# Kernel tuning notes

Measured on AMD Instinct MI355X. Metric: run time of the kernel, lower is better.

The kernel has to match this reference:

```python
import jax, jax.numpy as jnp
import numpy as np

ANCHORS_ALL = np.array([[10.,13.],[16.,30.],[33.,23.],[30.,61.],[62.,45.],
                        [59.,119.],[116.,90.],[156.,198.],[373.,326.]], np.float32)
ANCHORS_MASK = [0, 1, 2]
NUM_CLASS = 80
BBOX_ATTRIB = 5 + NUM_CLASS
IGNORE_THRES = 0.7
EPS = 1e-12


def _iou_cxcywh(a, b):
    ax1, ax2 = a[..., 0] - a[..., 2] / 2, a[..., 0] + a[..., 2] / 2
    ay1, ay2 = a[..., 1] - a[..., 3] / 2, a[..., 1] + a[..., 3] / 2
    bx1, bx2 = b[..., 0] - b[..., 2] / 2, b[..., 0] + b[..., 2] / 2
    by1, by2 = b[..., 1] - b[..., 3] / 2, b[..., 1] + b[..., 3] / 2
    iw = jnp.clip(jnp.minimum(ax2, bx2) - jnp.maximum(ax1, bx1), 0.0)
    ih = jnp.clip(jnp.minimum(ay2, by2) - jnp.maximum(ay1, by1), 0.0)
    inter = iw * ih
    union = a[..., 2] * a[..., 3] + b[..., 2] * b[..., 3] - inter
    return inter / (union + 1e-16)


def _build_targets(pred_boxes, target, anchors_all, anchors, nH, nW):
    # vectorized version of the per-(batch, gt-box) python double loop
    nB, nT, _ = target.shape
    nA = anchors.shape[0]
    # emulate `break` on first all-zero target row via cumulative validity
    valid = jnp.cumprod((target.sum(-1) != 0).astype(jnp.int32), axis=1).astype(bool)  # [B,T]
    gx, gy = target[..., 1] * nW, target[..., 2] * nH
    gw, gh = target[..., 3] * nW, target[..., 4] * nH
    gi = jnp.clip(gx.astype(jnp.int32), 0, nW - 1)
    gj = jnp.clip(gy.astype(jnp.int32), 0, nH - 1)
    gt_boxes = jnp.stack([gx, gy, gw, gh], -1)                                    # [B,T,4]
    # IoU of every GT against every predicted box -> ignore mask for noobj
    ious = _iou_cxcywh(pred_boxes.reshape(nB, 1, -1, 4), gt_boxes[:, :, None, :])  # [B,T,P]
    ignore = (ious > IGNORE_THRES) & valid[..., None]
    noobj_mask = 1.0 - jnp.any(ignore, axis=1).reshape(nB, nA, nH, nW).astype(jnp.float32)
    # anchor matching on w/h only (both boxes centered at origin)
    aw, ah = anchors_all[:, 0], anchors_all[:, 1]                                  # [9]
    inter = jnp.minimum(gw[..., None], aw) * jnp.minimum(gh[..., None], ah)
    union = gw[..., None] * gh[..., None] + aw * ah - inter
    best = jnp.argmax(inter / (union + 1e-16), axis=-1)                            # [B,T]
    lut = -np.ones(len(ANCHORS_ALL), np.int32)
    lut[np.array(ANCHORS_MASK)] = np.arange(nA, dtype=np.int32)
    a_loc = jnp.asarray(lut)[best]
    write = valid & (a_loc >= 0)                # only GTs whose best anchor is in this head's mask
    a_loc = jnp.clip(a_loc, 0)
    b_idx = jnp.where(write, jnp.arange(nB)[:, None], nB)   # route masked-out writes to dummy row nB
    coord_v = jnp.sqrt(2.0 - target[..., 3] * target[..., 4])
    tw_v = jnp.log(gw / anchors[a_loc, 0] + 1e-16)
    th_v = jnp.log(gh / anchors[a_loc, 1] + 1e-16)
    cls_i = jnp.clip(target[..., 0].astype(jnp.int32), 0, NUM_CLASS - 1)

    def scat(vals):
        return jnp.zeros((nB + 1, nA, nH, nW), jnp.float32).at[b_idx, a_loc, gj, gi].set(vals)[:nB]

    obj_mask = scat(jnp.ones_like(gx))
    box_coord_mask = scat(coord_v)
    tx = scat(gx - gi)
    ty = scat(gy - gj)
    tw = scat(tw_v)
    th = scat(th_v)
    tcls = (jnp.zeros((nB + 1, nA, nH, nW, NUM_CLASS), jnp.float32)
            .at[b_idx, a_loc, gj, gi, cls_i].set(1.0)[:nB])
    return obj_mask, noobj_mask, box_coord_mask, obj_mask, tcls, tx, ty, tw, th


def _bce_sum(p, t):
    return -jnp.sum(t * jnp.log(p + EPS) + (1.0 - t) * jnp.log(1.0 - p + EPS))


def _forward(x, target, img_dim):
    nB, _, nH, nW = x.shape
    nA = len(ANCHORS_MASK)
    stride = img_dim / nH
    anchors_all = jnp.asarray(ANCHORS_ALL) / stride
    anchors = anchors_all[jnp.asarray(ANCHORS_MASK)]
    preds = x.reshape(nB, nA, BBOX_ATTRIB, nH, nW).transpose(0, 1, 3, 4, 2)  # [B,A,H,W,85]
    preds_xy = jax.nn.sigmoid(preds[..., :2])
    preds_wh = preds[..., 2:4]
    preds_conf = jax.nn.sigmoid(preds[..., 4])
    preds_cls = jax.nn.sigmoid(preds[..., 5:])
    mesh_xy = jnp.stack(jnp.meshgrid(jnp.arange(nW, dtype=jnp.float32),
                                     jnp.arange(nH, dtype=jnp.float32)), -1)  # [H,W,2] = (x,y)
    # decoded boxes are detached in the original (used only to build targets)
    pred_boxes = jnp.concatenate(
        [jax.lax.stop_gradient(preds_xy) + mesh_xy,
         jnp.exp(jax.lax.stop_gradient(preds_wh)) * anchors[None, :, None, None, :]], -1)
    tgt = jax.lax.stop_gradient(target)  # target.detach() in original
    (obj_mask, noobj_mask, box_coord_mask, tconf, tcls,
     tx, ty, tw, th) = _build_targets(pred_boxes, tgt, anchors_all, anchors, nH, nW)
    mse = lambda a, b: jnp.sum((a - b) ** 2)
    loss_x = mse(preds_xy[..., 0] * box_coord_mask, tx * box_coord_mask) / 2
    loss_y = mse(preds_xy[..., 1] * box_coord_mask, ty * box_coord_mask) / 2
    loss_w = mse(preds_wh[..., 0] * box_coord_mask, tw * box_coord_mask) / 2
    loss_h = mse(preds_wh[..., 1] * box_coord_mask, th * box_coord_mask) / 2
    loss_conf = (_bce_sum(preds_conf * obj_mask, obj_mask)
                 + _bce_sum(preds_conf * noobj_mask, jnp.zeros_like(preds_conf)))
    # BCE over cls entries of object cells only (sum reduction) == mask-weighted sum
    loss_cls = -jnp.sum(obj_mask[..., None] * (tcls * jnp.log(preds_cls + EPS)
                                               + (1.0 - tcls) * jnp.log(1.0 - preds_cls + EPS)))
    return loss_x + loss_y + loss_w + loss_h + loss_conf + loss_cls


def setup_inputs() -> dict:
    key = jax.random.key(0)
    k1, k2, k3, k4 = jax.random.split(key, 4)
    nB, nT = 16, 50
    x = jax.random.normal(k1, (nB, 3 * BBOX_ATTRIB, 76, 76), jnp.float32)
    cls = jnp.floor(jax.random.uniform(k2, (nB, nT, 1)) * NUM_CLASS)
    cxy = jax.random.uniform(k3, (nB, nT, 2), minval=0.05, maxval=0.95)
    wh = jax.random.uniform(k4, (nB, nT, 2), minval=0.02, maxval=0.4)
    target = jnp.concatenate([cls, cxy, wh], -1).astype(jnp.float32)
    return {"x": x, "target": target, "img_dim": 608}


def reference(x, target, img_dim):
    return _forward(x, target, img_dim)
```

## Files before the change

### kernel.cpp

```cpp
#include <hip/hip_runtime.h>

#define NBATCH 16
#define NTGT   50
#define NA     3
#define NH     76
#define NW     76
#define HW     (NH*NW)
#define NC     80
#define NATT   85
#define CELLS  (NA*HW)
#define CBLK   68
#define BPB    (CBLK + 1)
#define NPART  (BPB * NBATCH)

__device__ __constant__ float c_anchors[18] = {
  10.f,13.f, 16.f,30.f, 33.f,23.f, 30.f,61.f, 62.f,45.f,
  59.f,119.f, 116.f,90.f, 156.f,198.f, 373.f,326.f };

__device__ inline float read_dim(const void* p) {
  int iv = *(const int*)p;
  if (iv > 0 && iv < (1 << 24)) return (float)iv;
  return *(const float*)p;
}

__launch_bounds__(256)
__global__ void yolo_all(const float* __restrict__ x,
                         const float* __restrict__ tgt,
                         const void*  __restrict__ dimp,
                         float*       __restrict__ wsf) {
  __shared__ float4 sbox[NTGT];
  __shared__ float  sarea[NTGT];
  __shared__ int    skey[NTGT];
  __shared__ int    scl [NTGT];
  __shared__ int    snv;
  __shared__ float  sred[4];

  int b   = blockIdx.y;
  int bx  = blockIdx.x;
  int tid = threadIdx.x;
  float istride = (float)NH / read_dim(dimp);

  float gx = 0.f, gy = 0.f, gw = 0.f, gh = 0.f, w = 0.f, h = 0.f;
  int   gi = 0, gj = 0, a = 0, mykey = -1;
  if (tid < 64) {
    float cls = 0.f, cx = 0.f, cy = 0.f, s = 1.f;
    if (tid < NTGT) {
      const float* tr = tgt + (size_t)(b * NTGT + tid) * 5;
      cls = tr[0]; cx = tr[1]; cy = tr[2]; w = tr[3]; h = tr[4];
      s = cls + cx + cy + w + h;
    }
    unsigned long long mz = __ballot(tid < NTGT && s == 0.0f);
    int nv = mz ? (__ffsll(mz) - 1) : NTGT;

    gx = cx * NW; gy = cy * NH; gw = w * NW; gh = h * NH;
    gi = min(max((int)gx, 0), NW - 1);
    gj = min(max((int)gy, 0), NH - 1);

    float best_r = -1.0f; int best = 0;
    for (int k = 0; k < 9; k++) {
      float aw = c_anchors[2*k] * istride, ah = c_anchors[2*k+1] * istride;
      float inter = fminf(gw, aw) * fminf(gh, ah);
      float uni   = gw * gh + aw * ah - inter;
      float r = inter / (uni + 1e-16f);
      if (r > best_r) { best_r = r; best = k; }
    }
    a = (best < NA) ? best : 0;
    mykey = (tid < nv && best < NA) ? (a * HW + gj * NW + gi) : -1;

    if (tid < NTGT) {
      sbox[tid]  = make_float4(gx - gw*0.5f, gx + gw*0.5f,
                               gy - gh*0.5f, gy + gh*0.5f);
      sarea[tid] = gw * gh;
      skey[tid]  = mykey;
      scl [tid]  = min(max((int)cls, 0), NC - 1);
    }
    if (tid == 0) snv = nv;
  }
  __syncthreads();

  float loss = 0.0f;
  int nv = snv;

  if (bx < CBLK) {
    int cell = bx * 256 + tid;
    if (cell < CELLS) {
      int ca  = cell / HW;
      int rem = cell - ca * HW;
      int j   = rem / NW;
      int i   = rem - j * NW;
      const float* xb = x + ((size_t)(b * NA + ca) * NATT) * HW + rem;
      float px = xb[0*HW], py = xb[1*HW], pw = xb[2*HW], ph = xb[3*HW], pc = xb[4*HW];
      float spx   = 1.0f / (1.0f + __expf(-px));
      float spy   = 1.0f / (1.0f + __expf(-py));
      float sconf = 1.0f / (1.0f + __expf(-pc));
      float bw = __expf(pw) * c_anchors[2*ca]   * istride;
      float bh = __expf(ph) * c_anchors[2*ca+1] * istride;
      float bxc = spx + (float)i, byc = spy + (float)j;
      float ax1 = bxc - bw * 0.5f, ax2 = bxc + bw * 0.5f;
      float ay1 = byc - bh * 0.5f, ay2 = byc + bh * 0.5f;
      float areaA = bw * bh;

      bool ign = false;
      for (int t = 0; t < nv; t++) {
        float4 bb = sbox[t];
        float iw = fmaxf(fminf(ax2, bb.y) - fmaxf(ax1, bb.x), 0.0f);
        float ih = fmaxf(fminf(ay2, bb.w) - fmaxf(ay1, bb.z), 0.0f);
        float inter = iw * ih;
        float uni   = areaA + sarea[t] - inter + 1e-16f;
        ign = ign | (inter > 0.7f * uni);
      }
      if (!ign) loss = -__logf(1.0f - sconf + 1e-12f);
    }
  } else if (tid < 64 && mykey >= 0) {
    bool winner = true;
    unsigned cb0 = 0, cb1 = 0, cb2 = 0;
    for (int t2 = 0; t2 < nv; t2++) {
      if (skey[t2] == mykey) {
        if (t2 > tid) winner = false;
        int c = scl[t2];
        if (c < 32)      cb0 |= (1u << c);
        else if (c < 64) cb1 |= (1u << (c - 32));
        else             cb2 |= (1u << (c - 64));
      }
    }
    if (winner) {
      const float* xb = x + ((size_t)(b * NA + a) * NATT) * HW + gj * NW + gi;
      float px = xb[0*HW], py = xb[1*HW], pw = xb[2*HW], ph = xb[3*HW], pc = xb[4*HW];
      float spx   = 1.0f / (1.0f + __expf(-px));
      float spy   = 1.0f / (1.0f + __expf(-py));
      float sconf = 1.0f / (1.0f + __expf(-pc));
      float aw = c_anchors[2*a] * istride, ah = c_anchors[2*a+1] * istride;
      loss += -__logf(sconf + 1e-12f);
      float m  = sqrtf(2.0f - w * h);
      float dx = (spx - (gx - (float)gi)) * m;
      float dy = (spy - (gy - (float)gj)) * m;
      float dw = (pw  - __logf(gw / aw + 1e-16f)) * m;
      float dh = (ph  - __logf(gh / ah + 1e-16f)) * m;
      loss += 0.5f * (dx*dx + dy*dy + dw*dw + dh*dh);
      for (int c = 0; c < NC; c++) {
        float pv = 1.0f / (1.0f + __expf(-xb[(5 + c) * HW]));
        bool on = (c < 32) ? ((cb0 >> c) & 1u)
                : (c < 64) ? ((cb1 >> (c - 32)) & 1u)
                           : ((cb2 >> (c - 64)) & 1u);
        loss += on ? -__logf(pv + 1e-12f) : -__logf(1.0f - pv + 1e-12f);
      }
    }
  }

  for (int off = 32; off > 0; off >>= 1) loss += __shfl_down(loss, off, 64);
  int wave = tid >> 6, lane = tid & 63;
  if (lane == 0) sred[wave] = loss;
  __syncthreads();
  if (tid == 0) wsf[b * BPB + bx] = sred[0] + sred[1] + sred[2] + sred[3];
}

__global__ void yolo_reduce(const float* __restrict__ wsf,
                            float*       __restrict__ out) {
  __shared__ float sred[4];
  int tid = threadIdx.x;
  float s = 0.0f;
  for (int i = tid; i < NPART; i += 256) s += wsf[i];
  for (int off = 32; off > 0; off >>= 1) s += __shfl_down(s, off, 64);
  int wave = tid >> 6, lane = tid & 63;
  if (lane == 0) sred[wave] = s;
  __syncthreads();
  if (tid == 0) out[0] = sred[0] + sred[1] + sred[2] + sred[3];
}

extern "C" void kernel_launch(void* const* d_in, const int* in_sizes, int n_in,
                              void* d_out, int out_size, void* d_ws, size_t ws_size,
                              hipStream_t stream) {
  const float* x    = (const float*)d_in[0];
  const float* tgt  = (const float*)d_in[1];
  const void*  dimp = d_in[2];
  float* out = (float*)d_out;
  float* wsf = (float*)d_ws;

  dim3 grid(BPB, NBATCH);
  yolo_all<<<grid, 256, 0, stream>>>(x, tgt, dimp, wsf);
  yolo_reduce<<<1, 256, 0, stream>>>(wsf, out);
}
```

Baseline: 150.9 us.

## Process four cells per thread with float4 loads in the noobj IoU pass

Each thread now handles four consecutive grid cells, loading predictions with float4 vector loads. Each target box read from shared memory is reused across four cells in the ignore-IoU loop. The number of cell blocks per batch drops accordingly. This amortizes LDS reads and loop overhead and adds ILP, at the cost of far fewer waves per CU and more registers.

New measurement: 149.1 us. About the same (-1.1%).

```diff
diff --git a/kernel.cpp b/kernel.cpp
--- a/kernel.cpp
+++ b/kernel.cpp
@@ -9,7 +9,7 @@
 #define NC     80
 #define NATT   85
 #define CELLS  (NA*HW)
-#define CBLK   68
+#define CBLK   17
 #define BPB    (CBLK + 1)
 #define NPART  (BPB * NBATCH)
 
@@ -82,34 +82,50 @@
   int nv = snv;
 
   if (bx < CBLK) {
-    int cell = bx * 256 + tid;
-    if (cell < CELLS) {
-      int ca  = cell / HW;
-      int rem = cell - ca * HW;
-      int j   = rem / NW;
-      int i   = rem - j * NW;
+    int base = bx * 1024 + tid * 4;
+    if (base < CELLS) {
+      int ca  = base / HW;
+      int rem = base - ca * HW;
       const float* xb = x + ((size_t)(b * NA + ca) * NATT) * HW + rem;
-      float px = xb[0*HW], py = xb[1*HW], pw = xb[2*HW], ph = xb[3*HW], pc = xb[4*HW];
-      float spx   = 1.0f / (1.0f + __expf(-px));
-      float spy   = 1.0f / (1.0f + __expf(-py));
-      float sconf = 1.0f / (1.0f + __expf(-pc));
-      float bw = __expf(pw) * c_anchors[2*ca]   * istride;
-      float bh = __expf(ph) * c_anchors[2*ca+1] * istride;
-      float bxc = spx + (float)i, byc = spy + (float)j;
-      float ax1 = bxc - bw * 0.5f, ax2 = bxc + bw * 0.5f;
-      float ay1 = byc - bh * 0.5f, ay2 = byc + bh * 0.5f;
-      float areaA = bw * bh;
+      float4 px4 = *(const float4*)(xb + 0*HW);
+      float4 py4 = *(const float4*)(xb + 1*HW);
+      float4 pw4 = *(const float4*)(xb + 2*HW);
+      float4 ph4 = *(const float4*)(xb + 3*HW);
+      float4 pc4 = *(const float4*)(xb + 4*HW);
+      float aw = c_anchors[2*ca] * istride, ah = c_anchors[2*ca+1] * istride;
 
-      bool ign = false;
+      float ax1[4], ax2[4], ay1[4], ay2[4], areaA[4], sconf[4];
+      #pragma unroll
+      for (int q = 0; q < 4; q++) {
+        int r2 = rem + q;
+        int j  = r2 / NW, i = r2 - j * NW;
+        float px = (&px4.x)[q], py = (&py4.x)[q];
+        float pw = (&pw4.x)[q], ph = (&ph4.x)[q], pc = (&pc4.x)[q];
+        float spx = 1.0f / (1.0f + __expf(-px));
+        float spy = 1.0f / (1.0f + __expf(-py));
+        sconf[q]  = 1.0f / (1.0f + __expf(-pc));
+        float bw = __expf(pw) * aw, bh = __expf(ph) * ah;
+        float bxc = spx + (float)i, byc = spy + (float)j;
+        ax1[q] = bxc - bw * 0.5f;  ax2[q] = bxc + bw * 0.5f;
+        ay1[q] = byc - bh * 0.5f;  ay2[q] = byc + bh * 0.5f;
+        areaA[q] = bw * bh;
+      }
+      bool ign[4] = {false, false, false, false};
       for (int t = 0; t < nv; t++) {
         float4 bb = sbox[t];
-        float iw = fmaxf(fminf(ax2, bb.y) - fmaxf(ax1, bb.x), 0.0f);
-        float ih = fmaxf(fminf(ay2, bb.w) - fmaxf(ay1, bb.z), 0.0f);
-        float inter = iw * ih;
-        float uni   = areaA + sarea[t] - inter + 1e-16f;
-        ign = ign | (inter > 0.7f * uni);
+        float sa  = sarea[t];
+        #pragma unroll
+        for (int q = 0; q < 4; q++) {
+          float iw = fmaxf(fminf(ax2[q], bb.y) - fmaxf(ax1[q], bb.x), 0.0f);
+          float ih = fmaxf(fminf(ay2[q], bb.w) - fmaxf(ay1[q], bb.z), 0.0f);
+          float inter = iw * ih;
+          float uni   = areaA[q] + sa - inter + 1e-16f;
+          ign[q] = ign[q] | (inter > 0.7f * uni);
+        }
       }
-      if (!ign) loss = -__logf(1.0f - sconf + 1e-12f);
+      #pragma unroll
+      for (int q = 0; q < 4; q++)
+        if (!ign[q]) loss += -__logf(1.0f - sconf[q] + 1e-12f);
     }
   } else if (tid < 64 && mykey >= 0) {
     bool winner = true;
```
